# Kernel optimization log

Measured on AMD Instinct MI355X. Metric: run time of the kernel, lower is better.

## Reference

```python
import jax, jax.numpy as jnp
import numpy as np
from jax import lax

N, IN_C, H, W = 8, 256, 100, 100
MID_C = 256
RATIOS = (0.5, 1.0, 2.0)
SCALES = (8, 16, 32)
FEAT_STRIDE = 16
BASE_SIZE = 16.0
K = len(RATIOS) * len(SCALES)
NMS_THRESH = 0.7
PRE_NMS = 3000
POST_NMS = 300
MIN_SIZE = 16.0


def _anchor_base():
    py = px = BASE_SIZE / 2.0
    ab = np.zeros((K, 4), np.float32)
    i = 0
    for r in RATIOS:
        for s in SCALES:
            h = BASE_SIZE * s * np.sqrt(r)
            w = BASE_SIZE * s * np.sqrt(1.0 / r)
            ab[i] = [py - h / 2.0, px - w / 2.0, py + h / 2.0, px + w / 2.0]
            i += 1
    return ab


def _all_anchors():
    ab = _anchor_base()
    sy = np.arange(H, dtype=np.float32) * FEAT_STRIDE
    sx = np.arange(W, dtype=np.float32) * FEAT_STRIDE
    yy, xx = np.meshgrid(sy, sx, indexing="ij")
    shifts = np.stack([yy.ravel(), xx.ravel(), yy.ravel(), xx.ravel()], 1)  # [HW,4]
    anchors = (shifts[:, None, :] + ab[None, :, :]).reshape(-1, 4)  # (h,w,k) order -> [K*H*W,4]
    return jnp.asarray(anchors)


def _conv(x, w, b, pad):
    y = lax.conv_general_dilated(x, w, (1, 1), [(pad, pad), (pad, pad)],
                                 dimension_numbers=("NCHW", "OIHW", "NCHW"))
    return y + b[None, :, None, None]


def _decode(anchors, loc):  # reg2bbox: boxes in [y1,x1,y2,x2], loc = [dy,dx,dh,dw]
    ah = anchors[:, 2] - anchors[:, 0]
    aw = anchors[:, 3] - anchors[:, 1]
    ay = anchors[:, 0] + 0.5 * ah
    ax = anchors[:, 1] + 0.5 * aw
    dy, dx, dh, dw = loc[:, 0], loc[:, 1], loc[:, 2], loc[:, 3]
    cy = dy * ah + ay
    cx = dx * aw + ax
    h = jnp.exp(dh) * ah
    w = jnp.exp(dw) * aw
    return jnp.stack([cy - 0.5 * h, cx - 0.5 * w, cy + 0.5 * h, cx + 0.5 * w], 1)


def _greedy_nms(boxes, valid):  # boxes sorted by score desc; returns keep mask
    P = boxes.shape[0]
    y1, x1, y2, x2 = boxes[:, 0], boxes[:, 1], boxes[:, 2], boxes[:, 3]
    areas = (y2 - y1) * (x2 - x1)
    idx = jnp.arange(P)

    def body(i, keep):
        yy1 = jnp.maximum(y1[i], y1)
        xx1 = jnp.maximum(x1[i], x1)
        yy2 = jnp.minimum(y2[i], y2)
        xx2 = jnp.minimum(x2[i], x2)
        inter = jnp.maximum(yy2 - yy1, 0.0) * jnp.maximum(xx2 - xx1, 0.0)
        iou = inter / (areas[i] + areas - inter + 1e-9)
        suppress = (iou > NMS_THRESH) & (idx > i) & keep[i]
        return keep & (~suppress)

    return lax.fori_loop(0, P, body, valid)


def _propose(anchors, scores, loc, img_w, img_h):
    boxes = _decode(anchors, loc)
    y1 = jnp.clip(boxes[:, 0], 0.0, img_h)
    y2 = jnp.clip(boxes[:, 2], 0.0, img_h)
    x1 = jnp.clip(boxes[:, 1], 0.0, img_w)
    x2 = jnp.clip(boxes[:, 3], 0.0, img_w)
    boxes = jnp.stack([y1, x1, y2, x2], 1)
    big = ((y2 - y1) >= MIN_SIZE) & ((x2 - x1) >= MIN_SIZE)
    s = jnp.where(big, scores, -1.0)  # push filtered boxes to the bottom (softmax scores in [0,1])
    order = jnp.argsort(-s)[:PRE_NMS]
    b = boxes[order]
    v = big[order]
    keep = _greedy_nms(lax.stop_gradient(b), v)
    # kept boxes first, preserving score order (matches torchvision nms index order)
    rank = jnp.where(keep, jnp.arange(PRE_NMS), PRE_NMS + jnp.arange(PRE_NMS))
    sel = jnp.argsort(rank)[:POST_NMS]
    roi = b[sel] * keep[sel][:, None].astype(b.dtype)  # zero-pad suppressed slots
    return roi


def reference(x, w1, b1, wc, bc, wr, br, img_width, img_height):
    h = jax.nn.relu(_conv(x, w1, b1, 1))
    cls = _conv(h, wc, bc, 0)  # [N,2K,H,W]
    cls = jnp.transpose(cls, (0, 2, 3, 1)).reshape(N, -1, 2)  # [N,KHW,2]
    fg = jax.nn.softmax(cls, axis=-1)[:, :, 1]  # [N,KHW]
    cls_out = jnp.transpose(cls, (0, 2, 1))  # [N,2,KHW]
    reg = _conv(h, wr, br, 0)
    reg = jnp.transpose(reg, (0, 2, 3, 1)).reshape(N, -1, 4)  # [N,KHW,4]
    anchors = _all_anchors()
    rois = jax.vmap(_propose, in_axes=(None, 0, 0, None, None))(
        anchors, fg, reg, float(img_width), float(img_height))  # [N,POST_NMS,4]
    roi_inds = jnp.repeat(jnp.arange(N, dtype=jnp.float32), POST_NMS)
    return cls_out, reg, rois.reshape(-1, 4), roi_inds, anchors


def setup_inputs() -> dict:
    key = jax.random.key(0)
    ks = jax.random.split(key, 4)
    std = 0.01
    return {
        "x": jax.random.normal(ks[0], (N, IN_C, H, W), jnp.float32),
        "w1": std * jax.random.normal(ks[1], (MID_C, IN_C, 3, 3), jnp.float32),
        "b1": jnp.zeros((MID_C,), jnp.float32),
        "wc": std * jax.random.normal(ks[2], (2 * K, MID_C, 1, 1), jnp.float32),
        "bc": jnp.zeros((2 * K,), jnp.float32),
        "wr": std * jax.random.normal(ks[3], (4 * K, MID_C, 1, 1), jnp.float32),
        "br": jnp.zeros((4 * K,), jnp.float32),
        "img_width": 1600,
        "img_height": 1600,
    }
```

## Files before the change

### kernel.cpp

```cpp
#include <hip/hip_runtime.h>
#include <cstdint>
#include <math.h>

static constexpr int NB  = 8;
static constexpr int CC_ = 256;
static constexpr int HH  = 100, WW = 100, HW = 10000;
static constexpr int KA  = 9;
static constexpr int AN  = HW * KA;
static constexpr int PRE  = 3000;
static constexpr int POST = 300;
static constexpr int NW64 = 47;
static constexpr float NMS_T = 0.7f;

typedef _Float16 f16;
typedef _Float16 f16x8 __attribute__((ext_vector_type(8)));
typedef float f32x4 __attribute__((ext_vector_type(4)));

static constexpr size_t OUT_CLS  = 0;
static constexpr size_t OUT_REG  = 1440000;
static constexpr size_t OUT_ROIS = 4320000;
static constexpr size_t OUT_RIND = 4329600;
static constexpr size_t OUT_ANCH = 4332000;

static constexpr size_t WS_H     = 0;
static constexpr size_t WS_WT    = 81920000;
static constexpr size_t WS_W54   = WS_WT   + 2359296;
static constexpr size_t WS_BOXES = WS_W54  + 55296;
static constexpr size_t WS_KEYS  = WS_BOXES+ 11520000;
static constexpr size_t WS_SBOX  = WS_KEYS + 2880000;
static constexpr size_t WS_SVAL  = WS_SBOX + 384000;
static constexpr size_t WS_MASK  = WS_SVAL + 96000;

__device__ __constant__ float AHC[9] = {
  90.50966799187809f, 181.01933598375618f, 362.03867196751236f,
  128.f, 256.f, 512.f,
  181.01933598375618f, 362.03867196751236f, 724.0773439350247f };
__device__ __constant__ float AWC[9] = {
  181.01933598375618f, 362.03867196751236f, 724.0773439350247f,
  128.f, 256.f, 512.f,
  90.50966799187809f, 181.01933598375618f, 362.03867196751236f };

__global__ void k_prep_all(const float* __restrict__ w1, const float* __restrict__ wc,
                           const float* __restrict__ wr, f16* __restrict__ WH,
                           f16* __restrict__ WL, float* __restrict__ w54,
                           float* __restrict__ anch) {
  int t = blockIdx.x * 256 + threadIdx.x;
  if (t < 589824) {
    int cil = t & 7, co = (t >> 3) & 255, rr = t >> 11;
    int kq = rr & 3, kg = (rr >> 2) & 7, tap = rr >> 5;
    int ci = kg * 32 + kq * 8 + cil;
    float v = w1[((size_t)co * 256 + ci) * 9 + tap];
    f16 hi = (f16)v;
    float res = v - (float)hi;
    WH[t] = hi;
    WL[t] = (f16)(res * 2048.f);
  }
  if (t < 256 * 54) {
    int ci = t / 54, j = t % 54;
    w54[t] = (j < 18) ? wc[j * 256 + ci] : wr[(j - 18) * 256 + ci];
  }
  int u = t - 256 * 54;
  if (u >= 0 && u < AN) {
    int k = u % KA; int pp = u / KA; int y = pp / WW; int x = pp % WW;
    int ri = k / 3, si = k % 3;
    double scale = (double)(8 << si);
    double r = (ri == 0) ? 0.5 : ((ri == 1) ? 1.0 : 2.0);
    double hh = 16.0 * scale * sqrt(r);
    double ww = 16.0 * scale * sqrt(1.0 / r);
    double sy = y * 16.0, sx = x * 16.0;
    anch[(size_t)u * 4 + 0] = (float)(sy + 8.0 - hh * 0.5);
    anch[(size_t)u * 4 + 1] = (float)(sx + 8.0 - ww * 0.5);
    anch[(size_t)u * 4 + 2] = (float)(sy + 8.0 + hh * 0.5);
    anch[(size_t)u * 4 + 3] = (float)(sx + 8.0 + ww * 0.5);
  }
}

__global__ __launch_bounds__(256, 2) void k_conv3x3(const float* __restrict__ x,
    const f16* __restrict__ WH, const f16* __restrict__ WL,
    const float* __restrict__ b1, float* __restrict__ hout) {
  __shared__ __align__(16) f16 SX[2][2][4][180][8];
  const int tid = threadIdx.x;
  const int lane = tid & 63;
  const int w = tid >> 6;
  const int xt = blockIdx.x % 7, yt = blockIdx.x / 7;
  const int cotile = blockIdx.y;
  const int n = blockIdx.z;
  const int x0 = xt * 16, y0 = yt * 8;
  const int wy = (w & 1) * 4;
  const int wc = (w >> 1) * 64;
  const int xb = lane & 15, kh = lane >> 4;

  const int sp = tid;
  const bool s_on = sp < 180;
  const int s_r = sp / 18, s_c = sp % 18;
  const int gy = y0 - 1 + s_r, gx = x0 - 1 + s_c;
  const bool s_ok = s_on && gy >= 0 && gy < HH && gx >= 0 && gx < WW;
  const int s_goff = s_ok ? gy * WW + gx : 0;

  const float* xn = x + (size_t)n * CC_ * HW;

  f32x4 acc1[4][4], acc2[4][4];
  #pragma unroll
  for (int a = 0; a < 4; ++a)
    #pragma unroll
    for (int b = 0; b < 4; ++b) {
      acc1[a][b] = (f32x4){0.f, 0.f, 0.f, 0.f};
      acc2[a][b] = (f32x4){0.f, 0.f, 0.f, 0.f};
    }

  float xv[32];
  auto prefetch = [&](int kg2) {
    if (s_ok) {
      const float* bp = xn + (size_t)(kg2 * 32) * HW + s_goff;
      #pragma unroll
      for (int j = 0; j < 32; ++j) xv[j] = bp[(size_t)j * HW];
    } else {
      #pragma unroll
      for (int j = 0; j < 32; ++j) xv[j] = 0.f;
    }
  };
  auto commit = [&](int nb) {
    if (s_on) {
      #pragma unroll
      for (int q = 0; q < 4; ++q) {
        f16x8 H, L;
        #pragma unroll
        for (int j = 0; j < 8; ++j) {
          float v = xv[q * 8 + j];
          f16 hi = (f16)v;
          float res = v - (float)hi;
          H[j] = hi;
          L[j] = (f16)(res * 2048.f);
        }
        *(f16x8*)&SX[nb][0][q][sp][0] = H;
        *(f16x8*)&SX[nb][1][q][sp][0] = L;
      }
    }
  };

  prefetch(0);
  commit(0);
  __syncthreads();

  const int cob = cotile * 128 + wc;
  for (int kg = 0; kg < 8; ++kg) {
    const int buf = kg & 1;
    if (kg < 7) prefetch(kg + 1);
    #pragma unroll
    for (int ky = 0; ky < 3; ++ky) {
      #pragma unroll
      for (int kx = 0; kx < 3; ++kx) {
        const int tap = ky * 3 + kx;
        const size_t wbase = ((((size_t)tap * 8 + kg) * 4 + kh) * 256 + cob + xb) * 8;
        f16x8 ah[4], al[4], bh[4], bl[4];
        #pragma unroll
        for (int cf = 0; cf < 4; ++cf) {
          ah[cf] = *(const f16x8*)(WH + wbase + (size_t)cf * 128);
          al[cf] = *(const f16x8*)(WL + wbase + (size_t)cf * 128);
        }
        #pragma unroll
        for (int nf = 0; nf < 4; ++nf) {
          const int pixf = (wy + nf + ky) * 18 + xb + kx;
          bh[nf] = *(const f16x8*)&SX[buf][0][kh][pixf][0];
          bl[nf] = *(const f16x8*)&SX[buf][1][kh][pixf][0];
        }
        #pragma unroll
        for (int cf = 0; cf < 4; ++cf)
          #pragma unroll
          for (int nf = 0; nf < 4; ++nf) {
            acc1[cf][nf] = __builtin_amdgcn_mfma_f32_16x16x32_f16(ah[cf], bh[nf], acc1[cf][nf], 0, 0, 0);
            acc2[cf][nf] = __builtin_amdgcn_mfma_f32_16x16x32_f16(ah[cf], bl[nf], acc2[cf][nf], 0, 0, 0);
            acc2[cf][nf] = __builtin_amdgcn_mfma_f32_16x16x32_f16(al[cf], bh[nf], acc2[cf][nf], 0, 0, 0);
          }
      }
    }
    if (kg < 7) commit(buf ^ 1);
    __syncthreads();
  }

  const int xg = x0 + xb;
  #pragma unroll
  for (int cf = 0; cf < 4; ++cf)
    #pragma unroll
    for (int r = 0; r < 4; ++r) {
      const int co = cob + cf * 16 + kh * 4 + r;
      const float bias = b1[co];
      const size_t obase = (size_t)(n * CC_ + co) * HH;
      #pragma unroll
      for (int nf = 0; nf < 4; ++nf) {
        const int yg = y0 + wy + nf;
        if (yg < HH && xg < WW) {
          float v = fmaf(acc2[cf][nf][r], 0.00048828125f, acc1[cf][nf][r]) + bias;
          hout[(obase + yg) * WW + xg] = fmaxf(v, 0.f);
        }
      }
    }
}

__global__ __launch_bounds__(256) void k_heads(const float* __restrict__ hin,
    const float* __restrict__ w54, const float* __restrict__ bc, const float* __restrict__ br,
    const int* __restrict__ imw, const int* __restrict__ imh,
    float* __restrict__ cls_out, float* __restrict__ reg_out,
    float* __restrict__ boxes, unsigned int* __restrict__ keys) {
  int gid = blockIdx.x * 256 + threadIdx.x;
  if (gid >= NB * HW) return;
  int n = gid / HW, p = gid % HW;
  float cacc[18], racc[36];
  #pragma unroll
  for (int j = 0; j < 18; ++j) cacc[j] = 0.f;
  #pragma unroll
  for (int j = 0; j < 36; ++j) racc[j] = 0.f;
  const float* hp = hin + (size_t)n * CC_ * HW + p;
  #pragma unroll 8
  for (int ci = 0; ci < CC_; ++ci) {
    float hv = hp[(size_t)ci * HW];
    const float* wrow = w54 + ci * 54;
    #pragma unroll
    for (int j = 0; j < 18; ++j) cacc[j] = fmaf(hv, wrow[j], cacc[j]);
    #pragma unroll
    for (int j = 0; j < 36; ++j) racc[j] = fmaf(hv, wrow[18 + j], racc[j]);
  }
  const float imgW = (float)imw[0], imgH = (float)imh[0];
  const int y = p / WW, xq = p % WW;
  #pragma unroll
  for (int k = 0; k < 9; ++k) {
    float c0 = cacc[2 * k] + bc[2 * k];
    float c1 = cacc[2 * k + 1] + bc[2 * k + 1];
    int a = p * 9 + k;
    cls_out[(size_t)n * 2 * AN + a]      = c0;
    cls_out[(size_t)n * 2 * AN + AN + a] = c1;
    float t0 = racc[4 * k]     + br[4 * k];
    float t1 = racc[4 * k + 1] + br[4 * k + 1];
    float t2 = racc[4 * k + 2] + br[4 * k + 2];
    float t3 = racc[4 * k + 3] + br[4 * k + 3];
    size_t ro = ((size_t)n * AN + a) * 4;
    reg_out[ro] = t0; reg_out[ro + 1] = t1; reg_out[ro + 2] = t2; reg_out[ro + 3] = t3;
    float hk = AHC[k], wk = AWC[k];
    float cy = fmaf(t0, hk, y  * 16.f + 8.f);
    float cx = fmaf(t1, wk, xq * 16.f + 8.f);
    float bh = expf(t2) * hk, bw = expf(t3) * wk;
    float y1 = cy - 0.5f * bh, x1 = cx - 0.5f * bw;
    float y2 = cy + 0.5f * bh, x2 = cx + 0.5f * bw;
    y1 = fminf(fmaxf(y1, 0.f), imgH); y2 = fminf(fmaxf(y2, 0.f), imgH);
    x1 = fminf(fmaxf(x1, 0.f), imgW); x2 = fminf(fmaxf(x2, 0.f), imgW);
    bool valid = (y2 - y1 >= 16.f) && (x2 - x1 >= 16.f);
    boxes[ro] = y1; boxes[ro + 1] = x1; boxes[ro + 2] = y2; boxes[ro + 3] = x2;
    float dc = c1 - c0;
    unsigned u = __float_as_uint(dc);
    u = (u & 0x80000000u) ? ~u : (u | 0x80000000u);
    keys[(size_t)n * AN + a] = valid ? u : 0u;
  }
}

__global__ __launch_bounds__(1024) void k_select(const unsigned* __restrict__ keys,
    const float* __restrict__ boxes, float* __restrict__ sbox, int* __restrict__ sval) {
  __shared__ unsigned hist[4][1024];
  __shared__ unsigned long long cand[4096];
  __shared__ int sB1, sA1, sB2, scnt;
  const int t = threadIdx.x;
  const int n = blockIdx.x;
  const unsigned* kp = keys + (size_t)n * AN;
  for (int i = t; i < 4096; i += 1024) ((unsigned*)hist)[i] = 0;
  __syncthreads();
  const int rep = (t >> 6) & 3;
  for (int i = t; i < AN; i += 1024) atomicAdd(&hist[rep][kp[i] >> 22], 1u);
  __syncthreads();
  unsigned myc = hist[0][t] + hist[1][t] + hist[2][t] + hist[3][t];
  __syncthreads();
  hist[0][t] = myc;
  __syncthreads();
  for (int off = 1; off < 1024; off <<= 1) {
    unsigned add = (t + off < 1024) ? hist[0][t + off] : 0;
    __syncthreads();
    hist[0][t] += add;
    __syncthreads();
  }
  unsigned incl = hist[0][t];
  unsigned above = incl - myc;
  if (above < (unsigned)PRE && incl >= (unsigned)PRE && myc > 0) { sB1 = t; sA1 = (int)above; }
  __syncthreads();
  const int B1 = sB1, A1 = sA1;
  __syncthreads();
  hist[0][t] = 0;
  __syncthreads();
  for (int i = t; i < AN; i += 1024) {
    unsigned k32 = kp[i];
    if ((int)(k32 >> 22) == B1) atomicAdd(&hist[0][(k32 >> 12) & 1023u], 1u);
  }
  __syncthreads();
  myc = hist[0][t];
  __syncthreads();
  for (int off = 1; off < 1024; off <<= 1) {
    unsigned add = (t + off < 1024) ? hist[0][t + off] : 0;
    __syncthreads();
    hist[0][t] += add;
    __syncthreads();
  }
  incl = hist[0][t]; above = incl - myc;
  const int target = PRE - A1;
  if ((int)above < target && (int)incl >= target && myc > 0) sB2 = t;
  if (t == 0) scnt = 0;
  __syncthreads();
  const int B2 = sB2;
  for (int i = t; i < AN; i += 1024) {
    unsigned k32 = kp[i];
    int b1 = (int)(k32 >> 22);
    bool sel = (b1 > B1) || (b1 == B1 && (int)((k32 >> 12) & 1023u) >= B2);
    if (sel) {
      int pos = atomicAdd(&scnt, 1);
      if (pos < 4096)
        cand[pos] = ((unsigned long long)k32 << 32) | (unsigned long long)(0xFFFFFFFFu - (unsigned)i);
    }
  }
  __syncthreads();
  int cnt = scnt; if (cnt > 4096) cnt = 4096;
  for (int i = cnt + t; i < 4096; i += 1024) cand[i] = 0ull;
  __syncthreads();
  for (int k = 2; k <= 4096; k <<= 1) {
    for (int j = k >> 1; j > 0; j >>= 1) {
      for (int i = t; i < 4096; i += 1024) {
        int ixj = i ^ j;
        if (ixj > i) {
          unsigned long long va = cand[i], vb = cand[ixj];
          bool desc = ((i & k) == 0);
          if (desc ? (va < vb) : (va > vb)) { cand[i] = vb; cand[ixj] = va; }
        }
      }
      __syncthreads();
    }
  }
  for (int i = t; i < PRE; i += 1024) {
    unsigned long long kv = cand[i];
    unsigned idx = 0xFFFFFFFFu - (unsigned)(kv & 0xFFFFFFFFull);
    float4 bb = *(const float4*)(boxes + ((size_t)n * AN + idx) * 4);
    *(float4*)(sbox + ((size_t)n * PRE + i) * 4) = bb;
    sval[n * PRE + i] = ((kv >> 32) != 0ull) ? 1 : 0;
  }
}

__global__ __launch_bounds__(256) void k_mask(const float* __restrict__ sbox,
    unsigned long long* __restrict__ mask) {
  __shared__ float4 jb[64];
  const int t = threadIdx.x;
  const int lane = t & 63, wv = t >> 6;
  const int jt = blockIdx.x, n = blockIdx.z;
  const int it = blockIdx.y * 4 + wv;
  const int j0 = jt * 64;
  if (t < 64) {
    int jg = j0 + t;
    float4 v = make_float4(0.f, 0.f, 0.f, 0.f);
    if (jg < PRE) v = *(const float4*)(sbox + ((size_t)n * PRE + jg) * 4);
    jb[t] = v;
  }
  __syncthreads();
  const int i = it * 64 + lane;
  if (it >= NW64 || i >= PRE) return;
  float4 bi = *(const float4*)(sbox + ((size_t)n * PRE + i) * 4);
  float areaI = (bi.z - bi.x) * (bi.w - bi.y);
  unsigned long long bits = 0ull;
  #pragma unroll 4
  for (int jj = 0; jj < 64; ++jj) {
    int j = j0 + jj;
    float4 bj = jb[jj];
    float yy1 = fmaxf(bi.x, bj.x), xx1 = fmaxf(bi.y, bj.y);
    float yy2 = fminf(bi.z, bj.z), xx2 = fminf(bi.w, bj.w);
    float inter = fmaxf(yy2 - yy1, 0.f) * fmaxf(xx2 - xx1, 0.f);
    float areaJ = (bj.z - bj.x) * (bj.w - bj.y);
    float iou = inter / (areaI + areaJ - inter + 1e-9f);
    if (iou > NMS_T && j > i && j < PRE) bits |= (1ull << jj);
  }
  mask[((size_t)n * 3008 + i) * NW64 + jt] = bits;
}

__global__ __launch_bounds__(256) void k_nms_final(const unsigned long long* __restrict__ mask,
    const int* __restrict__ sval, const float* __restrict__ sbox,
    float* __restrict__ rois, float* __restrict__ rind) {
  __shared__ unsigned long long kws[NW64];
  __shared__ int pref[NW64 + 1];
  const int t = threadIdx.x, n = blockIdx.x;
  if (t < 64) {
    unsigned long long keep = 0ull;
    for (int w = 0; w < NW64; ++w) {
      int i = w * 64 + t;
      int v = (i < PRE) ? sval[n * PRE + i] : 0;
      unsigned long long m = __ballot(v != 0);
      if (t == w) keep = m;
    }
    const unsigned long long* mrow = mask + (size_t)n * 3008 * NW64;
    unsigned long long buf[16];
    #pragma unroll
    for (int r = 0; r < 16; ++r)
      buf[r] = (t < NW64) ? mrow[(size_t)r * NW64 + t] : 0ull;
    for (int base = 0; base < PRE; base += 16) {
      #pragma unroll
      for (int r = 0; r < 16; ++r) {
        int i = base + r;
        if (i < PRE) {
          unsigned long long kb = __shfl(keep, i >> 6);
          if ((kb >> (i & 63)) & 1ull) keep &= ~buf[r];
        }
        int nx = i + 16;
        buf[r] = (nx < PRE && t < NW64) ? mrow[(size_t)nx * NW64 + t] : 0ull;
      }
    }
    if (t < NW64) kws[t] = keep;
  }
  __syncthreads();
  if (t == 0) {
    int s = 0;
    for (int w = 0; w < NW64; ++w) { pref[w] = s; s += __popcll(kws[w]); }
    pref[NW64] = s;
  }
  for (int e = t; e < POST * 4; e += 256) rois[(size_t)n * POST * 4 + e] = 0.f;
  for (int e = t; e < POST; e += 256) rind[(size_t)n * POST + e] = (float)n;
  __syncthreads();
  for (int i = t; i < PRE; i += 256) {
    int wd = i >> 6, b = i & 63;
    unsigned long long wv = kws[wd];
    if ((wv >> b) & 1ull) {
      int rank = pref[wd] + __popcll(wv & ((1ull << b) - 1ull));
      if (rank < POST) {
        float4 bb = *(const float4*)(sbox + ((size_t)n * PRE + i) * 4);
        *(float4*)(rois + ((size_t)n * POST + rank) * 4) = bb;
      }
    }
  }
}

extern "C" void kernel_launch(void* const* d_in, const int* in_sizes, int n_in,
                              void* d_out, int out_size, void* d_ws, size_t ws_size,
                              hipStream_t stream) {
  const float* x  = (const float*)d_in[0];
  const float* w1 = (const float*)d_in[1];
  const float* b1 = (const float*)d_in[2];
  const float* wc = (const float*)d_in[3];
  const float* bc = (const float*)d_in[4];
  const float* wr = (const float*)d_in[5];
  const float* br = (const float*)d_in[6];
  const int* imw  = (const int*)d_in[7];
  const int* imh  = (const int*)d_in[8];
  float* out = (float*)d_out;
  char* ws = (char*)d_ws;
  float* hbuf = (float*)(ws + WS_H);
  f16* WH     = (f16*)(ws + WS_WT);
  f16* WL     = (f16*)(ws + WS_WT + 1179648);
  float* w54  = (float*)(ws + WS_W54);
  float* boxes = (float*)(ws + WS_BOXES);
  unsigned* keys = (unsigned*)(ws + WS_KEYS);
  float* sbox = (float*)(ws + WS_SBOX);
  int* sval   = (int*)(ws + WS_SVAL);
  unsigned long long* mask  = (unsigned long long*)(ws + WS_MASK);

  k_prep_all<<<2304, 256, 0, stream>>>(w1, wc, wr, WH, WL, w54, out + OUT_ANCH);
  k_conv3x3<<<dim3(91, 2, NB), 256, 0, stream>>>(x, WH, WL, b1, hbuf);
  k_heads<<<313, 256, 0, stream>>>(hbuf, w54, bc, br, imw, imh,
                                   out + OUT_CLS, out + OUT_REG, boxes, keys);
  k_select<<<NB, 1024, 0, stream>>>(keys, boxes, sbox, sval);
  k_mask<<<dim3(NW64, 12, NB), 256, 0, stream>>>(sbox, mask);
  k_nms_final<<<NB, 256, 0, stream>>>(mask, sval, sbox, out + OUT_ROIS, out + OUT_RIND);
}
```

Baseline: 1.305 ms.

## Halve conv output-channel tile per block and split input prefetch to cut registers

The 3x3 conv block now covers 64 output channels instead of 128, and the grid's channel dimension doubles to keep coverage. The next channel group is staged in two 16-channel halves, with the first half committed mid-tap loop. Together these shrink accumulator and prefetch registers so launch bounds can ask for 3 blocks per SM, and one padding element is added to the shared array. In exchange, each input tile is loaded and converted twice as often across blocks, lowering data reuse per weight fetch.

```diff
diff --git a/kernel.cpp b/kernel.cpp
--- a/kernel.cpp
+++ b/kernel.cpp
@@ -75,10 +75,10 @@
   }
 }
 
-__global__ __launch_bounds__(256, 2) void k_conv3x3(const float* __restrict__ x,
+__global__ __launch_bounds__(256, 3) void k_conv3x3(const float* __restrict__ x,
     const f16* __restrict__ WH, const f16* __restrict__ WL,
     const float* __restrict__ b1, float* __restrict__ hout) {
-  __shared__ __align__(16) f16 SX[2][2][4][180][8];
+  __shared__ __align__(16) f16 SX[2][2][4][181][8];
   const int tid = threadIdx.x;
   const int lane = tid & 63;
   const int w = tid >> 6;
@@ -87,7 +87,7 @@
   const int n = blockIdx.z;
   const int x0 = xt * 16, y0 = yt * 8;
   const int wy = (w & 1) * 4;
-  const int wc = (w >> 1) * 64;
+  const int wc = (w >> 1) * 32;
   const int xb = lane & 15, kh = lane >> 4;
 
   const int sp = tid;
@@ -99,30 +99,30 @@
 
   const float* xn = x + (size_t)n * CC_ * HW;
 
-  f32x4 acc1[4][4], acc2[4][4];
+  f32x4 acc1[2][4], acc2[2][4];
   #pragma unroll
-  for (int a = 0; a < 4; ++a)
+  for (int a = 0; a < 2; ++a)
     #pragma unroll
     for (int b = 0; b < 4; ++b) {
       acc1[a][b] = (f32x4){0.f, 0.f, 0.f, 0.f};
       acc2[a][b] = (f32x4){0.f, 0.f, 0.f, 0.f};
     }
 
-  float xv[32];
-  auto prefetch = [&](int kg2) {
+  float xv[16];
+  auto prefetch16 = [&](int kg2, int half) {
     if (s_ok) {
-      const float* bp = xn + (size_t)(kg2 * 32) * HW + s_goff;
-      #pragma unroll
-      for (int j = 0; j < 32; ++j) xv[j] = bp[(size_t)j * HW];
+      const float* bp = xn + (size_t)(kg2 * 32 + half * 16) * HW + s_goff;
+      #pragma unroll
+      for (int j = 0; j < 16; ++j) xv[j] = bp[(size_t)j * HW];
     } else {
       #pragma unroll
-      for (int j = 0; j < 32; ++j) xv[j] = 0.f;
+      for (int j = 0; j < 16; ++j) xv[j] = 0.f;
     }
   };
-  auto commit = [&](int nb) {
+  auto commit16 = [&](int nb, int half) {
     if (s_on) {
       #pragma unroll
-      for (int q = 0; q < 4; ++q) {
+      for (int q = 0; q < 2; ++q) {
         f16x8 H, L;
         #pragma unroll
         for (int j = 0; j < 8; ++j) {
@@ -132,55 +132,57 @@
           H[j] = hi;
           L[j] = (f16)(res * 2048.f);
         }
-        *(f16x8*)&SX[nb][0][q][sp][0] = H;
-        *(f16x8*)&SX[nb][1][q][sp][0] = L;
+        *(f16x8*)&SX[nb][0][half * 2 + q][sp][0] = H;
+        *(f16x8*)&SX[nb][1][half * 2 + q][sp][0] = L;
       }
     }
   };
 
-  prefetch(0);
-  commit(0);
-  __syncthreads();
-
-  const int cob = cotile * 128 + wc;
+  prefetch16(0, 0); commit16(0, 0);
+  prefetch16(0, 1); commit16(0, 1);
+  __syncthreads();
+
+  const int cob = cotile * 64 + wc;
   for (int kg = 0; kg < 8; ++kg) {
     const int buf = kg & 1;
-    if (kg < 7) prefetch(kg + 1);
-    #pragma unroll
-    for (int ky = 0; ky < 3; ++ky) {
-      #pragma unroll
-      for (int kx = 0; kx < 3; ++kx) {
-        const int tap = ky * 3 + kx;
-        const size_t wbase = ((((size_t)tap * 8 + kg) * 4 + kh) * 256 + cob + xb) * 8;
-        f16x8 ah[4], al[4], bh[4], bl[4];
-        #pragma unroll
-        for (int cf = 0; cf < 4; ++cf) {
-          ah[cf] = *(const f16x8*)(WH + wbase + (size_t)cf * 128);
-          al[cf] = *(const f16x8*)(WL + wbase + (size_t)cf * 128);
-        }
+    const bool more = (kg < 7);
+    if (more) prefetch16(kg + 1, 0);
+    #pragma unroll
+    for (int t9 = 0; t9 < 9; ++t9) {
+      const int ky = t9 / 3, kx = t9 % 3;
+      const size_t wbase = ((((size_t)t9 * 8 + kg) * 4 + kh) * 256 + cob + xb) * 8;
+      f16x8 ah[2], al[2], bh[4], bl[4];
+      #pragma unroll
+      for (int cf = 0; cf < 2; ++cf) {
+        ah[cf] = *(const f16x8*)(WH + wbase + (size_t)cf * 128);
+        al[cf] = *(const f16x8*)(WL + wbase + (size_t)cf * 128);
+      }
+      #pragma unroll
+      for (int nf = 0; nf < 4; ++nf) {
+        const int pixf = (wy + nf + ky) * 18 + xb + kx;
+        bh[nf] = *(const f16x8*)&SX[buf][0][kh][pixf][0];
+        bl[nf] = *(const f16x8*)&SX[buf][1][kh][pixf][0];
+      }
+      #pragma unroll
+      for (int cf = 0; cf < 2; ++cf)
         #pragma unroll
         for (int nf = 0; nf < 4; ++nf) {
-          const int pixf = (wy + nf + ky) * 18 + xb + kx;
-          bh[nf] = *(const f16x8*)&SX[buf][0][kh][pixf][0];
-          bl[nf] = *(const f16x8*)&SX[buf][1][kh][pixf][0];
+          acc1[cf][nf] = __builtin_amdgcn_mfma_f32_16x16x32_f16(ah[cf], bh[nf], acc1[cf][nf], 0, 0, 0);
+          acc2[cf][nf] = __builtin_amdgcn_mfma_f32_16x16x32_f16(ah[cf], bl[nf], acc2[cf][nf], 0, 0, 0);
+          acc2[cf][nf] = __builtin_amdgcn_mfma_f32_16x16x32_f16(al[cf], bh[nf], acc2[cf][nf], 0, 0, 0);
         }
-        #pragma unroll
-        for (int cf = 0; cf < 4; ++cf)
-          #pragma unroll
-          for (int nf = 0; nf < 4; ++nf) {
-            acc1[cf][nf] = __builtin_amdgcn_mfma_f32_16x16x32_f16(ah[cf], bh[nf], acc1[cf][nf], 0, 0, 0);
-            acc2[cf][nf] = __builtin_amdgcn_mfma_f32_16x16x32_f16(ah[cf], bl[nf], acc2[cf][nf], 0, 0, 0);
-            acc2[cf][nf] = __builtin_amdgcn_mfma_f32_16x16x32_f16(al[cf], bh[nf], acc2[cf][nf], 0, 0, 0);
-          }
-      }
-    }
-    if (kg < 7) commit(buf ^ 1);
+      if (t9 == 3 && more) {
+        commit16(buf ^ 1, 0);
+        prefetch16(kg + 1, 1);
+      }
+    }
+    if (more) commit16(buf ^ 1, 1);
     __syncthreads();
   }
 
   const int xg = x0 + xb;
   #pragma unroll
-  for (int cf = 0; cf < 4; ++cf)
+  for (int cf = 0; cf < 2; ++cf)
     #pragma unroll
     for (int r = 0; r < 4; ++r) {
       const int co = cob + cf * 16 + kh * 4 + r;
@@ -452,7 +454,7 @@
   unsigned long long* mask  = (unsigned long long*)(ws + WS_MASK);
 
   k_prep_all<<<2304, 256, 0, stream>>>(w1, wc, wr, WH, WL, w54, out + OUT_ANCH);
-  k_conv3x3<<<dim3(91, 2, NB), 256, 0, stream>>>(x, WH, WL, b1, hbuf);
+  k_conv3x3<<<dim3(91, 4, NB), 256, 0, stream>>>(x, WH, WL, b1, hbuf);
   k_heads<<<313, 256, 0, stream>>>(hbuf, w54, bc, br, imw, imh,
                                    out + OUT_CLS, out + OUT_REG, boxes, keys);
   k_select<<<NB, 1024, 0, stream>>>(keys, boxes, sbox, sval);
```

Measured after the change: 1.290 ms. Within noise of the previous version (-1.2%).
